# Optimization experiments

Measured on AMD Instinct MI355X. Metric: run time of the kernel, lower is better.

Reference implementation:

```python
import jax, jax.numpy as jnp
import numpy as np

B, C, REP, H, W = 4, 256, 128, 32, 128
EPS = 1e-5


def _conv1x1(x, w, b=None):
    # x: [B, Cin, H, W], w: [Cout, Cin]
    y = jnp.einsum('oc,bchw->bohw', w, x)
    if b is not None:
        y = y + b[None, :, None, None]
    return y


def _bn_train(x, gamma, beta):
    # BatchNorm2d in training mode: batch stats over (B, H, W)
    mean = jnp.mean(x, axis=(0, 2, 3), keepdims=True)
    var = jnp.var(x, axis=(0, 2, 3), keepdims=True)
    xn = (x - mean) * jax.lax.rsqrt(var + EPS)
    return gamma[None, :, None, None] * xn + beta[None, :, None, None]


def setup_inputs() -> dict:
    key = jax.random.key(0)
    ks = jax.random.split(key, 20)
    f = lambda k, s: jax.random.normal(k, s, dtype=jnp.float32)
    inp = {
        'left': f(ks[0], (B, C, H, W)),
        'right': f(ks[1], (B, C, H, W)),
        'pre_l': jax.random.uniform(ks[2], (B, 1, H, W), dtype=jnp.float32) * W,
        'pre_r': jax.random.uniform(ks[3], (B, 1, H, W), dtype=jnp.float32) * W,
        'query_l': f(ks[4], (B, REP, H, W)),
        'key_l': f(ks[5], (B, REP, H, W)),
        'query_r': f(ks[6], (B, REP, H, W)),
        'key_r': f(ks[7], (B, REP, H, W)),
        # learned 1x1-conv params (kernel stored as [Cout, Cin])
        'theta_w': f(ks[8], (REP, C + 1)) * 0.02,
        'theta_b': f(ks[9], (REP,)) * 0.02,
        'phi_w': f(ks[10], (REP, C)) * 0.02,
        'phi_b': f(ks[11], (REP,)) * 0.02,
        'g_w': f(ks[12], (REP, C)) * 0.02,
        'g_b': f(ks[13], (REP,)) * 0.02,
        'up_w': f(ks[14], (C, REP)) * 0.02,
        'up_b': f(ks[15], (C,)) * 0.02,
        'bn_gamma': f(ks[16], (C,)) * 0.1 + 1.0,
        'bn_beta': f(ks[17], (C,)) * 0.1,
    }
    return inp


def _side(x_q, x_kv, pre, query, key_feat,
          theta_w, theta_b, phi_w, phi_b, g_w, g_b,
          up_w, up_b, bn_gamma, bn_beta):
    hw = H * W
    pre = pre / W
    # theta: [B, hw, REP]
    theta = _conv1x1(jnp.concatenate([x_q, pre], axis=1), theta_w, theta_b)
    theta = theta.reshape(B, REP, hw).transpose(0, 2, 1) + \
        query.reshape(B, REP, hw).transpose(0, 2, 1)
    # phi: [B, REP, hw]
    phi = _conv1x1(x_kv, phi_w, phi_b).reshape(B, REP, hw) + \
        key_feat.reshape(B, REP, hw)
    # g: [B, hw, REP]
    g = _conv1x1(x_kv, g_w, g_b).reshape(B, REP, hw).transpose(0, 2, 1)
    # attention over all hw key positions: [B, hw, hw]
    atten = jax.nn.softmax(jnp.einsum('bqc,bck->bqk', theta, phi), axis=-1)
    # soft-argmax over key column index (arange(W) tiled H times along key axis)
    col_idx = jnp.tile(jnp.arange(W, dtype=jnp.float32), H)  # [hw]
    exp_col = jnp.einsum('bqk,k->bq', atten, col_idx)        # [B, hw]
    q_col = (jnp.arange(hw, dtype=jnp.float32) % W)[None, :]  # [1, hw]
    index = (q_col - exp_col).reshape(B, H, W)
    # value aggregation + residual projection
    after = jnp.einsum('bqk,bkc->bqc', atten, g)
    after = after.transpose(0, 2, 1).reshape(B, REP, H, W)
    out = x_q + _bn_train(_conv1x1(after, up_w, up_b), bn_gamma, bn_beta)
    return out, index


def reference(left, right, pre_l, pre_r, query_l, key_l, query_r, key_r,
              theta_w, theta_b, phi_w, phi_b, g_w, g_b,
              up_w, up_b, bn_gamma, bn_beta):
    l_n, index_l = _side(left, right, pre_l, query_l, key_r,
                         theta_w, theta_b, phi_w, phi_b, g_w, g_b,
                         up_w, up_b, bn_gamma, bn_beta)
    r_n, index_r = _side(right, left, pre_r, query_r, key_l,
                         theta_w, theta_b, phi_w, phi_b, g_w, g_b,
                         up_w, up_b, bn_gamma, bn_beta)
    return (l_n, r_n, index_l, index_r)
```

## Files before the change

### kernel.cpp

```cpp
#include <hip/hip_runtime.h>


typedef unsigned short u16;
typedef unsigned int   u32;
typedef float        floatx4 __attribute__((ext_vector_type(4)));
typedef unsigned int uintx4  __attribute__((ext_vector_type(4)));
typedef unsigned int uintx2  __attribute__((ext_vector_type(2)));
typedef _Float16     half8   __attribute__((ext_vector_type(8)));
typedef __fp16       fp16x2  __attribute__((ext_vector_type(2)));

#define HW 4096
#define CB 256
#define RP 128
#define EPSF 1e-5f

static __device__ __forceinline__ u16 f2bf(float f) {
  u32 u = __float_as_uint(f);
  u32 r = u + 0x7FFFu + ((u >> 16) & 1u);
  return (u16)(r >> 16);
}
static __device__ __forceinline__ float bf2f(u16 h) {
  return __uint_as_float(((u32)h) << 16);
}
static __device__ __forceinline__ u16 f2h(float f) {
  _Float16 h = (_Float16)f;
  return __builtin_bit_cast(u16, h);
}
static __device__ __forceinline__ float h2f(u16 h) {
  return (float)__builtin_bit_cast(_Float16, h);
}
static __device__ __forceinline__ half8 as_h8(uintx4 v) {
  return __builtin_bit_cast(half8, v);
}
static __device__ __forceinline__ u32 pkrtz(float a, float b) {
  fp16x2 h = __builtin_amdgcn_cvt_pkrtz(a, b);
  return __builtin_bit_cast(u32, h);
}
static __device__ __forceinline__ u32 pk2h(float a, float b) {
  return (u32)f2h(a) | ((u32)f2h(b) << 16);
}
static __device__ __forceinline__ void barrier_nodrain() {
  __builtin_amdgcn_sched_barrier(0);
  asm volatile("s_waitcnt lgkmcnt(0)" ::: "memory");
  __builtin_amdgcn_s_barrier();
  __builtin_amdgcn_sched_barrier(0);
}

union Pk4 { u16 u[4]; uintx2 v; };

struct ProjCfg {
  const float* x; const float* w; const float* bias;
  const float* add; const float* pre; u16* out;
  int wstride; int transposed;
};
struct ProjCfg6 { ProjCfg c[6]; };

#define XSTR 40

__global__ __launch_bounds__(256) void ra_projm(ProjCfg6 cfg, float* stz)
{
  __shared__ u16 x_lds[128 * XSTR];
  __shared__ u16 w_lds[128 * XSTR];
  if (blockIdx.x == 0) {
    ((floatx4*)stz)[threadIdx.x] = (floatx4)0.0f;
  }
  const ProjCfg C = cfg.c[blockIdx.x >> 7];
  const int inner = blockIdx.x & 127;
  const int b    = inner >> 5;
  const int pos0 = (inner & 31) * 128;
  const int tid  = threadIdx.x;
  const int wv   = tid >> 6;
  const int lane = tid & 63;
  const int ln16 = lane & 15;
  const int quad = lane >> 4;
  const int mbase = wv * 32;

  const int xc0 = (tid & 7) * 4, xp0 = (tid >> 3) * 4;
  const int wrr = tid >> 1, wch = (tid & 1) * 16;
  const bool walign = (C.wstride & 3) == 0;

  floatx4 acc[2][8];
  #pragma unroll
  for (int mt = 0; mt < 2; mt++)
    #pragma unroll
    for (int nt = 0; nt < 8; nt++) acc[mt][nt] = (floatx4)0.0f;

  floatx4 xr[4];
  floatx4 ww4[4];
  {
    #pragma unroll
    for (int i = 0; i < 4; i++)
      xr[i] = *(const floatx4*)(C.x + (size_t)(b * CB + xc0 + i) * HW + pos0 + xp0);
    const float* wp = C.w + (size_t)wrr * C.wstride + wch;
    if (walign) {
      #pragma unroll
      for (int i = 0; i < 4; i++) ww4[i] = *(const floatx4*)(wp + i * 4);
    } else {
      #pragma unroll
      for (int i = 0; i < 4; i++)
        #pragma unroll
        for (int jj = 0; jj < 4; jj++) ww4[i][jj] = wp[i * 4 + jj];
    }
  }

  #pragma unroll 1
  for (int cc = 0; cc < 8; ++cc) {
    barrier_nodrain();
    #pragma unroll
    for (int pp = 0; pp < 4; pp++) {
      uintx2 v;
      v[0] = pk2h(xr[0][pp], xr[1][pp]);
      v[1] = pk2h(xr[2][pp], xr[3][pp]);
      *(uintx2*)&x_lds[(xp0 + pp) * XSTR + xc0] = v;
    }
    {
      uintx4 v0, v1;
      v0[0] = pk2h(ww4[0][0], ww4[0][1]); v0[1] = pk2h(ww4[0][2], ww4[0][3]);
      v0[2] = pk2h(ww4[1][0], ww4[1][1]); v0[3] = pk2h(ww4[1][2], ww4[1][3]);
      v1[0] = pk2h(ww4[2][0], ww4[2][1]); v1[1] = pk2h(ww4[2][2], ww4[2][3]);
      v1[2] = pk2h(ww4[3][0], ww4[3][1]); v1[3] = pk2h(ww4[3][2], ww4[3][3]);
      *(uintx4*)&w_lds[wrr * XSTR + wch]     = v0;
      *(uintx4*)&w_lds[wrr * XSTR + wch + 8] = v1;
    }
    if (cc < 7) {
      const int c2 = (cc + 1) * 32;
      #pragma unroll
      for (int i = 0; i < 4; i++)
        xr[i] = *(const floatx4*)(C.x + (size_t)(b * CB + c2 + xc0 + i) * HW + pos0 + xp0);
      const float* wp = C.w + (size_t)wrr * C.wstride + c2 + wch;
      if (walign) {
        #pragma unroll
        for (int i = 0; i < 4; i++) ww4[i] = *(const floatx4*)(wp + i * 4);
      } else {
        #pragma unroll
        for (int i = 0; i < 4; i++)
          #pragma unroll
          for (int jj = 0; jj < 4; jj++) ww4[i][jj] = wp[i * 4 + jj];
      }
    }
    barrier_nodrain();
    if (!C.transposed) {
      half8 a0 = as_h8(*(const uintx4*)&w_lds[(mbase + ln16) * XSTR + quad * 8]);
      half8 a1 = as_h8(*(const uintx4*)&w_lds[(mbase + 16 + ln16) * XSTR + quad * 8]);
      #pragma unroll
      for (int nt = 0; nt < 8; nt++) {
        half8 bf = as_h8(*(const uintx4*)&x_lds[(nt * 16 + ln16) * XSTR + quad * 8]);
        acc[0][nt] = __builtin_amdgcn_mfma_f32_16x16x32_f16(a0, bf, acc[0][nt], 0, 0, 0);
        acc[1][nt] = __builtin_amdgcn_mfma_f32_16x16x32_f16(a1, bf, acc[1][nt], 0, 0, 0);
      }
    } else {
      half8 a0 = as_h8(*(const uintx4*)&x_lds[(mbase + ln16) * XSTR + quad * 8]);
      half8 a1 = as_h8(*(const uintx4*)&x_lds[(mbase + 16 + ln16) * XSTR + quad * 8]);
      #pragma unroll
      for (int nt = 0; nt < 8; nt++) {
        half8 bf = as_h8(*(const uintx4*)&w_lds[(nt * 16 + ln16) * XSTR + quad * 8]);
        acc[0][nt] = __builtin_amdgcn_mfma_f32_16x16x32_f16(a0, bf, acc[0][nt], 0, 0, 0);
        acc[1][nt] = __builtin_amdgcn_mfma_f32_16x16x32_f16(a1, bf, acc[1][nt], 0, 0, 0);
      }
    }
  }

  if (!C.transposed) {
    #pragma unroll
    for (int mt = 0; mt < 2; mt++) {
      const int r0 = mbase + mt * 16 + quad * 4;
      floatx4 bi = *(const floatx4*)(C.bias + r0);
      float wc[4];
      if (C.pre) {
        #pragma unroll
        for (int rr = 0; rr < 4; rr++) wc[rr] = C.w[(size_t)(r0 + rr) * C.wstride + 256];
      }
      #pragma unroll
      for (int nt = 0; nt < 8; nt++) {
        const int pos = pos0 + nt * 16 + ln16;
        floatx4 v = acc[mt][nt];
        #pragma unroll
        for (int rr = 0; rr < 4; rr++) v[rr] += bi[rr];
        if (C.pre) {
          const float pv = C.pre[(size_t)b * HW + pos] * (1.f / 128.f);
          #pragma unroll
          for (int rr = 0; rr < 4; rr++) v[rr] += pv * wc[rr];
        }
        if (C.add) {
          #pragma unroll
          for (int rr = 0; rr < 4; rr++)
            v[rr] += C.add[(size_t)(b * RP + r0 + rr) * HW + pos];
        }
        Pk4 pk;
        #pragma unroll
        for (int rr = 0; rr < 4; rr++) pk.u[rr] = f2h(v[rr]);
        *(uintx2*)(C.out + (size_t)(b * HW + pos) * RP + r0) = pk.v;
      }
    }
  } else {
    #pragma unroll
    for (int nt = 0; nt < 8; nt++) {
      const int r = nt * 16 + ln16;
      const float bs = C.bias[r];
      #pragma unroll
      for (int mt = 0; mt < 2; mt++) {
        const int pv = pos0 + mbase + mt * 16 + quad * 4;
        floatx4 v = acc[mt][nt];
        Pk4 pk;
        #pragma unroll
        for (int rr = 0; rr < 4; rr++) pk.u[rr] = f2h(v[rr] + bs);
        *(uintx2*)(C.out + (size_t)(b * RP + r) * HW + pv) = pk.v;
      }
    }
  }
}

__global__ __launch_bounds__(256) void ra_flash(
    const u16* __restrict__ thetaL, const u16* __restrict__ phiTL,
    const u16* __restrict__ gTL,
    const u16* __restrict__ thetaR, const u16* __restrict__ phiTR,
    const u16* __restrict__ gTR,
    u16* __restrict__ afterL, u16* __restrict__ afterR,
    float* __restrict__ idxL, float* __restrict__ idxR)
{
  __shared__ uintx4 phi_lds[16 * 65];
  __shared__ uintx4 g_lds[8 * 129];
  __shared__ u16 P_lds[4][16 * 76];

  const int tid  = threadIdx.x;
  const int bx   = blockIdx.x;
  const int side = bx >> 8;
  const int sbx  = bx & 255;
  const u16* __restrict__ theta = side ? thetaR : thetaL;
  const u16* __restrict__ phiT  = side ? phiTR  : phiTL;
  const u16* __restrict__ gT    = side ? gTR    : gTL;

  const int b    = sbx >> 6;
  const int q0   = (sbx & 63) * 64;
  const int wv   = tid >> 6;
  const int lane = tid & 63;
  const int ln16 = lane & 15;
  const int quad = lane >> 4;

  uintx4 aq[4];
  {
    const uintx4* tr = (const uintx4*)(theta + (size_t)(b * HW + q0 + wv * 16 + ln16) * RP);
    #pragma unroll
    for (int c = 0; c < 4; c++) aq[c] = tr[c * 4 + quad];
  }

  half8 cf0, cf1;
  {
    #pragma unroll
    for (int i = 0; i < 8; i++) {
      float c0 = (ln16 == 0) ? (float)(quad * 8 + i)      : (ln16 == 1 ? 1.f : 0.f);
      float c1 = (ln16 == 0) ? (float)(32 + quad * 8 + i) : (ln16 == 1 ? 1.f : 0.f);
      cf0[i] = (_Float16)c0;
      cf1[i] = (_Float16)c1;
    }
  }

  floatx4 accO[8];
  #pragma unroll
  for (int v = 0; v < 8; v++) accO[v] = (floatx4)0.0f;
  floatx4 accE  = (floatx4)0.0f;
  floatx4 accEo = (floatx4)0.0f;
  float m_q = -3.0e38f;

  const int sk  = tid >> 4, scb = tid & 15;
  const int gv_ = tid >> 3, gcb = tid & 7;

  uintx4 sp[4], sg[4];
  #pragma unroll
  for (int i = 0; i < 4; i++) {
    sp[i] = *(const uintx4*)(phiT + (size_t)(b * HW + i * 16 + sk) * RP + scb * 8);
    sg[i] = *(const uintx4*)(gT + (size_t)(b * RP + i * 32 + gv_) * HW + gcb * 8);
  }

  #pragma unroll 1
  for (int j = 0; j < 64; j++) {
    #pragma unroll
    for (int i = 0; i < 4; i++) {
      phi_lds[scb * 65 + i * 16 + sk] = sp[i];
      g_lds[gcb * 129 + i * 32 + gv_] = sg[i];
    }
    if (j < 63) {
      const int k0n = (j + 1) * 64;
      #pragma unroll
      for (int i = 0; i < 4; i++) {
        sp[i] = *(const uintx4*)(phiT + (size_t)(b * HW + k0n + i * 16 + sk) * RP + scb * 8);
        sg[i] = *(const uintx4*)(gT + (size_t)(b * RP + i * 32 + gv_) * HW + k0n + gcb * 8);
      }
    }
    barrier_nodrain();

    floatx4 sf[4];
    #pragma unroll
    for (int s = 0; s < 4; s++) sf[s] = (floatx4)0.0f;
    __builtin_amdgcn_s_setprio(1);
    #pragma unroll
    for (int c = 0; c < 4; c++) {
      half8 bth = as_h8(aq[c]);
      #pragma unroll
      for (int s = 0; s < 4; s++) {
        uintx4 ap = phi_lds[(c * 4 + quad) * 65 + s * 16 + ln16];
        sf[s] = __builtin_amdgcn_mfma_f32_16x16x32_f16(as_h8(ap), bth, sf[s], 0, 0, 0);
      }
    }
    __builtin_amdgcn_s_setprio(0);

    float ms0 = fmaxf(fmaxf(sf[0][0], sf[0][1]), fmaxf(sf[0][2], sf[0][3]));
    float ms1 = fmaxf(fmaxf(sf[1][0], sf[1][1]), fmaxf(sf[1][2], sf[1][3]));
    float ms2 = fmaxf(fmaxf(sf[2][0], sf[2][1]), fmaxf(sf[2][2], sf[2][3]));
    float ms3 = fmaxf(fmaxf(sf[3][0], sf[3][1]), fmaxf(sf[3][2], sf[3][3]));
    float mx = fmaxf(fmaxf(ms0, ms1), fmaxf(ms2, ms3));
    mx = fmaxf(mx, __shfl_xor(mx, 16));
    mx = fmaxf(mx, __shfl_xor(mx, 32));
    if (__any(mx > m_q + 8.f)) {
      const float mnew  = fmaxf(m_q, mx);
      const float alpha = __expf(m_q - mnew);
      m_q = mnew;
      accE *= alpha; accEo *= alpha;
      #pragma unroll
      for (int v = 0; v < 8; v++) accO[v] *= alpha;
    }
    #pragma unroll
    for (int s = 0; s < 4; s++) {
      float p0 = __expf(sf[s][0] - m_q);
      float p1 = __expf(sf[s][1] - m_q);
      float p2 = __expf(sf[s][2] - m_q);
      float p3 = __expf(sf[s][3] - m_q);
      uintx2 pkv;
      pkv[0] = pkrtz(p0, p1);
      pkv[1] = pkrtz(p2, p3);
      *(uintx2*)&P_lds[wv][ln16 * 76 + s * 16 + quad * 4] = pkv;
    }

    half8 pb0 = as_h8(*(const uintx4*)&P_lds[wv][ln16 * 76 + quad * 8]);
    half8 pb1 = as_h8(*(const uintx4*)&P_lds[wv][ln16 * 76 + 32 + quad * 8]);
    __builtin_amdgcn_s_setprio(1);
    #pragma unroll
    for (int vt = 0; vt < 8; vt++) {
      uintx4 ag0 = g_lds[quad * 129 + vt * 16 + ln16];
      uintx4 ag1 = g_lds[(4 + quad) * 129 + vt * 16 + ln16];
      accO[vt] = __builtin_amdgcn_mfma_f32_16x16x32_f16(as_h8(ag0), pb0, accO[vt], 0, 0, 0);
      accO[vt] = __builtin_amdgcn_mfma_f32_16x16x32_f16(as_h8(ag1), pb1, accO[vt], 0, 0, 0);
    }
    if (j & 1) {
      accEo = __builtin_amdgcn_mfma_f32_16x16x32_f16(cf0, pb0, accEo, 0, 0, 0);
      accEo = __builtin_amdgcn_mfma_f32_16x16x32_f16(cf1, pb1, accEo, 0, 0, 0);
    } else {
      accE  = __builtin_amdgcn_mfma_f32_16x16x32_f16(cf0, pb0, accE, 0, 0, 0);
      accE  = __builtin_amdgcn_mfma_f32_16x16x32_f16(cf1, pb1, accE, 0, 0, 0);
    }
    __builtin_amdgcn_s_setprio(0);
    barrier_nodrain();
  }

  const float l0 = accE[1] + accEo[1];
  const float a0 = accE[0] + accEo[0] + 64.f * accEo[1];
  const float l_all  = __shfl(l0, ln16);
  const float aC_all = __shfl(a0, ln16);

  const int q = q0 + wv * 16 + ln16;
  const size_t p = (size_t)b * HW + q;
  u16* after = side ? afterR : afterL;
  u16* orow = after + p * RP;
  const float invl = 1.f / l_all;
  #pragma unroll
  for (int vt = 0; vt < 8; vt++) {
    uintx2 pkv;
    pkv[0] = pkrtz(accO[vt][0] * invl, accO[vt][1] * invl);
    pkv[1] = pkrtz(accO[vt][2] * invl, accO[vt][3] * invl);
    *(uintx2*)(orow + vt * 16 + quad * 4) = pkv;
  }
  if (quad == 0) {
    float* idx = side ? idxR : idxL;
    idx[p] = (float)(q & 127) - aC_all * invl;
  }
}

#define WSTR 136

__global__ __launch_bounds__(256) void ra_upm(
    const u16* __restrict__ afterL, const u16* __restrict__ afterR,
    const float* __restrict__ w, const float* __restrict__ bias,
    u16* __restrict__ yL, u16* __restrict__ yR,
    float* __restrict__ stL, float* __restrict__ stR)
{
  __shared__ u16 w_lds[128 * WSTR];
  const int tid  = threadIdx.x;
  const int bx   = blockIdx.x;
  const int side = bx >> 8;
  const int sbx  = bx & 255;
  const u16* __restrict__ after = side ? afterR : afterL;
  u16* __restrict__ y = side ? yR : yL;
  const int b    = sbx >> 6;
  const int pos0 = ((sbx >> 1) & 31) * 128;
  const int hc   = sbx & 1;
  const int wv   = tid >> 6;
  const int lane = tid & 63;
  const int ln16 = lane & 15;
  const int quad = lane >> 4;

  {
    const int co = tid >> 1, rh = (tid & 1) * 64;
    const float* wp = w + (size_t)(hc * 128 + co) * RP + rh;
    #pragma unroll
    for (int i = 0; i < 8; i++) {
      floatx4 f0 = *(const floatx4*)(wp + i * 8);
      floatx4 f1 = *(const floatx4*)(wp + i * 8 + 4);
      uintx4 v;
      v[0] = pk2h(f0[0], f0[1]); v[1] = pk2h(f0[2], f0[3]);
      v[2] = pk2h(f1[0], f1[1]); v[3] = pk2h(f1[2], f1[3]);
      *(uintx4*)&w_lds[co * WSTR + rh + i * 8] = v;
    }
  }
  __syncthreads();

  floatx4 acc[2][8];
  #pragma unroll
  for (int mt = 0; mt < 2; mt++)
    #pragma unroll
    for (int nt = 0; nt < 8; nt++) acc[mt][nt] = (floatx4)0.0f;

  #pragma unroll
  for (int kk = 0; kk < 4; kk++) {
    half8 a[2];
    #pragma unroll
    for (int mt = 0; mt < 2; mt++)
      a[mt] = as_h8(*(const uintx4*)(after +
          (size_t)(b * HW + pos0 + wv * 32 + mt * 16 + ln16) * RP + kk * 32 + quad * 8));
    #pragma unroll
    for (int nt = 0; nt < 8; nt++) {
      half8 bf = as_h8(*(const uintx4*)&w_lds[(nt * 16 + ln16) * WSTR + kk * 32 + quad * 8]);
      acc[0][nt] = __builtin_amdgcn_mfma_f32_16x16x32_f16(a[0], bf, acc[0][nt], 0, 0, 0);
      acc[1][nt] = __builtin_amdgcn_mfma_f32_16x16x32_f16(a[1], bf, acc[1][nt], 0, 0, 0);
    }
  }

  float s_nt[8], q_nt[8];
  #pragma unroll
  for (int nt = 0; nt < 8; nt++) {
    const int co = hc * 128 + nt * 16 + ln16;
    const float bs = bias[co];
    float s = 0.f, sq = 0.f;
    #pragma unroll
    for (int mt = 0; mt < 2; mt++) {
      const int pv = pos0 + wv * 32 + mt * 16 + quad * 4;
      floatx4 v = acc[mt][nt];
      Pk4 pk;
      #pragma unroll
      for (int rr = 0; rr < 4; rr++) {
        const float yv = v[rr] + bs;
        s += yv; sq += yv * yv;
        pk.u[rr] = f2bf(yv);
      }
      *(uintx2*)(y + (size_t)(b * CB + co) * HW + pv) = pk.v;
    }
    s  += __shfl_xor(s, 16);  s  += __shfl_xor(s, 32);
    sq += __shfl_xor(sq, 16); sq += __shfl_xor(sq, 32);
    s_nt[nt] = s; q_nt[nt] = sq;
  }
  __syncthreads();
  float* scr = (float*)w_lds;
  if (quad == 0) {
    #pragma unroll
    for (int nt = 0; nt < 8; nt++) {
      scr[wv * 128 + nt * 16 + ln16]       = s_nt[nt];
      scr[512 + wv * 128 + nt * 16 + ln16] = q_nt[nt];
    }
  }
  __syncthreads();
  if (tid < 128) {
    const float s  = scr[tid] + scr[128 + tid] + scr[256 + tid] + scr[384 + tid];
    const float sq = scr[512 + tid] + scr[640 + tid] + scr[768 + tid] + scr[896 + tid];
    float* stats = side ? stR : stL;
    atomicAdd(&stats[2 * (hc * 128 + tid)], s);
    atomicAdd(&stats[2 * (hc * 128 + tid) + 1], sq);
  }
}

__global__ __launch_bounds__(256) void ra_fin(
    const float* __restrict__ left, const float* __restrict__ right,
    const u16* __restrict__ yL, const u16* __restrict__ yR,
    const float* __restrict__ stL, const float* __restrict__ stR,
    const float* __restrict__ gamma, const float* __restrict__ beta,
    float* __restrict__ out)
{
  const size_t e = (size_t)blockIdx.x * 256 + threadIdx.x;
  const int side = (int)(e >> 20);
  const size_t e4 = e & 1048575;
  const int c = (int)((e4 >> 10) & 255);
  const float* x = side ? right : left;
  const u16* y = side ? yR : yL;
  const float* stats = side ? stR : stL;
  const float s = stats[2 * c], sq = stats[2 * c + 1];
  const float mean = s * (1.f / 16384.f);
  const float var  = sq * (1.f / 16384.f) - mean * mean;
  const float rstd = rsqrtf(var + EPSF);
  const float ga = gamma[c], be = beta[c];
  floatx4 xv = ((const floatx4*)x)[e4];
  uintx2 yv = ((const uintx2*)y)[e4];
  float f0 = bf2f((u16)(yv[0] & 0xffffu));
  float f1 = bf2f((u16)(yv[0] >> 16));
  float f2 = bf2f((u16)(yv[1] & 0xffffu));
  float f3 = bf2f((u16)(yv[1] >> 16));
  floatx4 o;
  o[0] = xv[0] + ga * ((f0 - mean) * rstd) + be;
  o[1] = xv[1] + ga * ((f1 - mean) * rstd) + be;
  o[2] = xv[2] + ga * ((f2 - mean) * rstd) + be;
  o[3] = xv[3] + ga * ((f3 - mean) * rstd) + be;
  ((floatx4*)out)[(size_t)side * 1048576 + e4] = o;
}

extern "C" void kernel_launch(void* const* d_in, const int* in_sizes, int n_in,
                              void* d_out, int out_size, void* d_ws, size_t ws_size,
                              hipStream_t stream)
{
  const float* left    = (const float*)d_in[0];
  const float* right   = (const float*)d_in[1];
  const float* pre_l   = (const float*)d_in[2];
  const float* pre_r   = (const float*)d_in[3];
  const float* query_l = (const float*)d_in[4];
  const float* key_l   = (const float*)d_in[5];
  const float* query_r = (const float*)d_in[6];
  const float* key_r   = (const float*)d_in[7];
  const float* theta_w = (const float*)d_in[8];
  const float* theta_b = (const float*)d_in[9];
  const float* phi_w   = (const float*)d_in[10];
  const float* phi_b   = (const float*)d_in[11];
  const float* g_w     = (const float*)d_in[12];
  const float* g_b     = (const float*)d_in[13];
  const float* up_w    = (const float*)d_in[14];
  const float* up_b    = (const float*)d_in[15];
  const float* bn_g    = (const float*)d_in[16];
  const float* bn_b    = (const float*)d_in[17];
  float* out = (float*)d_out;

  char* ws = (char*)d_ws;
  const size_t SZ = (size_t)4 * HW * RP * 2;
  u16* thetaL = (u16*)(ws);
  u16* phiTL  = (u16*)(ws + 1 * SZ);
  u16* gTL    = (u16*)(ws + 2 * SZ);
  u16* thetaR = (u16*)(ws + 3 * SZ);
  u16* phiTR  = (u16*)(ws + 4 * SZ);
  u16* gTR    = (u16*)(ws + 5 * SZ);
  u16* afterL = (u16*)(ws + 6 * SZ);
  u16* afterR = (u16*)(ws + 7 * SZ);
  u16* yL     = (u16*)(ws + 8 * SZ);
  u16* yR     = (u16*)(ws + 10 * SZ);
  float* stL  = (float*)(ws + 12 * SZ);
  float* stR  = (float*)(ws + 12 * SZ + 2048);

  dim3 blk(256);
  ProjCfg6 pc;
  pc.c[0] = { left,  theta_w, theta_b, query_l, pre_l,   thetaL, 257, 0 };
  pc.c[1] = { right, phi_w,   phi_b,   key_r,   nullptr, phiTL,  256, 0 };
  pc.c[2] = { right, g_w,     g_b,     nullptr, nullptr, gTL,    256, 1 };
  pc.c[3] = { right, theta_w, theta_b, query_r, pre_r,   thetaR, 257, 0 };
  pc.c[4] = { left,  phi_w,   phi_b,   key_l,   nullptr, phiTR,  256, 0 };
  pc.c[5] = { left,  g_w,     g_b,     nullptr, nullptr, gTR,    256, 1 };
  ra_projm<<<768, blk, 0, stream>>>(pc, stL);

  ra_flash<<<512, blk, 0, stream>>>(thetaL, phiTL, gTL, thetaR, phiTR, gTR,
                                    afterL, afterR,
                                    out + 8388608, out + 8404992);
  ra_upm<<<512, blk, 0, stream>>>(afterL, afterR, up_w, up_b, yL, yR, stL, stR);
  ra_fin<<<8192, blk, 0, stream>>>(left, right, yL, yR, stL, stR, bn_g, bn_b, out);

  (void)in_sizes; (void)n_in; (void)out_size; (void)ws_size;
}
```

Baseline: 312.6 us.

## Recompute up-projection in BN finalize instead of storing y; swizzle flash block order

The up-projection kernel now only accumulates the BatchNorm sum and sum-of-squares. The finalize kernel recomputes the 1x1-conv GEMM from the attention output and applies the normalization and residual directly. This removes the bf16 y intermediate write and its re-read, at the cost of doing the small GEMM twice. The flash kernel's block index is also permuted so that consecutive blocks are spread across sides and batches, which may improve L2 locality or load balance across XCDs.

```diff
diff --git a/kernel.cpp b/kernel.cpp
--- a/kernel.cpp
+++ b/kernel.cpp
@@ -223,7 +223,8 @@
   __shared__ u16 P_lds[4][16 * 76];
 
   const int tid  = threadIdx.x;
-  const int bx   = blockIdx.x;
+  const int h    = blockIdx.x;
+  const int bx   = ((h & 7) << 6) | (h >> 3);
   const int side = bx >> 8;
   const int sbx  = bx & 255;
   const u16* __restrict__ theta = side ? thetaR : thetaL;
@@ -377,10 +378,9 @@
 
 #define WSTR 136
 
-__global__ __launch_bounds__(256) void ra_upm(
+__global__ __launch_bounds__(256) void ra_upstats(
     const u16* __restrict__ afterL, const u16* __restrict__ afterR,
     const float* __restrict__ w, const float* __restrict__ bias,
-    u16* __restrict__ yL, u16* __restrict__ yR,
     float* __restrict__ stL, float* __restrict__ stR)
 {
   __shared__ u16 w_lds[128 * WSTR];
@@ -389,7 +389,6 @@
   const int side = bx >> 8;
   const int sbx  = bx & 255;
   const u16* __restrict__ after = side ? afterR : afterL;
-  u16* __restrict__ y = side ? yR : yL;
   const int b    = sbx >> 6;
   const int pos0 = ((sbx >> 1) & 31) * 128;
   const int hc   = sbx & 1;
@@ -437,21 +436,15 @@
   float s_nt[8], q_nt[8];
   #pragma unroll
   for (int nt = 0; nt < 8; nt++) {
-    const int co = hc * 128 + nt * 16 + ln16;
-    const float bs = bias[co];
+    const float bs = bias[hc * 128 + nt * 16 + ln16];
     float s = 0.f, sq = 0.f;
     #pragma unroll
     for (int mt = 0; mt < 2; mt++) {
-      const int pv = pos0 + wv * 32 + mt * 16 + quad * 4;
-      floatx4 v = acc[mt][nt];
-      Pk4 pk;
       #pragma unroll
       for (int rr = 0; rr < 4; rr++) {
-        const float yv = v[rr] + bs;
+        const float yv = acc[mt][nt][rr] + bs;
         s += yv; sq += yv * yv;
-        pk.u[rr] = f2bf(yv);
-      }
-      *(uintx2*)(y + (size_t)(b * CB + co) * HW + pv) = pk.v;
+      }
     }
     s  += __shfl_xor(s, 16);  s  += __shfl_xor(s, 32);
     sq += __shfl_xor(sq, 16); sq += __shfl_xor(sq, 32);
@@ -476,37 +469,89 @@
   }
 }
 
-__global__ __launch_bounds__(256) void ra_fin(
+__global__ __launch_bounds__(256) void ra_finm(
+    const u16* __restrict__ afterL, const u16* __restrict__ afterR,
+    const float* __restrict__ w, const float* __restrict__ bias,
     const float* __restrict__ left, const float* __restrict__ right,
-    const u16* __restrict__ yL, const u16* __restrict__ yR,
     const float* __restrict__ stL, const float* __restrict__ stR,
     const float* __restrict__ gamma, const float* __restrict__ beta,
     float* __restrict__ out)
 {
-  const size_t e = (size_t)blockIdx.x * 256 + threadIdx.x;
-  const int side = (int)(e >> 20);
-  const size_t e4 = e & 1048575;
-  const int c = (int)((e4 >> 10) & 255);
+  __shared__ u16 w_lds[128 * WSTR];
+  const int tid  = threadIdx.x;
+  const int bx   = blockIdx.x;
+  const int side = bx >> 8;
+  const int sbx  = bx & 255;
+  const u16* __restrict__ after = side ? afterR : afterL;
+  const int b    = sbx >> 6;
+  const int pos0 = ((sbx >> 1) & 31) * 128;
+  const int hc   = sbx & 1;
+  const int wv   = tid >> 6;
+  const int lane = tid & 63;
+  const int ln16 = lane & 15;
+  const int quad = lane >> 4;
+
+  {
+    const int co = tid >> 1, rh = (tid & 1) * 64;
+    const float* wp = w + (size_t)(hc * 128 + co) * RP + rh;
+    #pragma unroll
+    for (int i = 0; i < 8; i++) {
+      floatx4 f0 = *(const floatx4*)(wp + i * 8);
+      floatx4 f1 = *(const floatx4*)(wp + i * 8 + 4);
+      uintx4 v;
+      v[0] = pk2h(f0[0], f0[1]); v[1] = pk2h(f0[2], f0[3]);
+      v[2] = pk2h(f1[0], f1[1]); v[3] = pk2h(f1[2], f1[3]);
+      *(uintx4*)&w_lds[co * WSTR + rh + i * 8] = v;
+    }
+  }
+  __syncthreads();
+
+  floatx4 acc[2][8];
+  #pragma unroll
+  for (int mt = 0; mt < 2; mt++)
+    #pragma unroll
+    for (int nt = 0; nt < 8; nt++) acc[mt][nt] = (floatx4)0.0f;
+
+  #pragma unroll
+  for (int kk = 0; kk < 4; kk++) {
+    half8 a[2];
+    #pragma unroll
+    for (int mt = 0; mt < 2; mt++)
+      a[mt] = as_h8(*(const uintx4*)(after +
+          (size_t)(b * HW + pos0 + wv * 32 + mt * 16 + ln16) * RP + kk * 32 + quad * 8));
+    #pragma unroll
+    for (int nt = 0; nt < 8; nt++) {
+      half8 bf = as_h8(*(const uintx4*)&w_lds[(nt * 16 + ln16) * WSTR + kk * 32 + quad * 8]);
+      acc[0][nt] = __builtin_amdgcn_mfma_f32_16x16x32_f16(a[0], bf, acc[0][nt], 0, 0, 0);
+      acc[1][nt] = __builtin_amdgcn_mfma_f32_16x16x32_f16(a[1], bf, acc[1][nt], 0, 0, 0);
+    }
+  }
+
   const float* x = side ? right : left;
-  const u16* y = side ? yR : yL;
   const float* stats = side ? stR : stL;
-  const float s = stats[2 * c], sq = stats[2 * c + 1];
-  const float mean = s * (1.f / 16384.f);
-  const float var  = sq * (1.f / 16384.f) - mean * mean;
-  const float rstd = rsqrtf(var + EPSF);
-  const float ga = gamma[c], be = beta[c];
-  floatx4 xv = ((const floatx4*)x)[e4];
-  uintx2 yv = ((const uintx2*)y)[e4];
-  float f0 = bf2f((u16)(yv[0] & 0xffffu));
-  float f1 = bf2f((u16)(yv[0] >> 16));
-  float f2 = bf2f((u16)(yv[1] & 0xffffu));
-  float f3 = bf2f((u16)(yv[1] >> 16));
-  floatx4 o;
-  o[0] = xv[0] + ga * ((f0 - mean) * rstd) + be;
-  o[1] = xv[1] + ga * ((f1 - mean) * rstd) + be;
-  o[2] = xv[2] + ga * ((f2 - mean) * rstd) + be;
-  o[3] = xv[3] + ga * ((f3 - mean) * rstd) + be;
-  ((floatx4*)out)[(size_t)side * 1048576 + e4] = o;
+  float* outs = out + (size_t)side * 4194304;
+  #pragma unroll
+  for (int nt = 0; nt < 8; nt++) {
+    const int co = hc * 128 + nt * 16 + ln16;
+    const float s = stats[2 * co], sq = stats[2 * co + 1];
+    const float mean = s * (1.f / 16384.f);
+    const float var  = sq * (1.f / 16384.f) - mean * mean;
+    const float rstd = rsqrtf(var + EPSF);
+    const float ga = gamma[co], be = beta[co];
+    const float bs = bias[co];
+    #pragma unroll
+    for (int mt = 0; mt < 2; mt++) {
+      const int pv = pos0 + wv * 32 + mt * 16 + quad * 4;
+      floatx4 xv = *(const floatx4*)(x + (size_t)(b * CB + co) * HW + pv);
+      floatx4 o;
+      #pragma unroll
+      for (int rr = 0; rr < 4; rr++) {
+        const float yv = acc[mt][nt][rr] + bs;
+        o[rr] = xv[rr] + ga * ((yv - mean) * rstd) + be;
+      }
+      *(floatx4*)(outs + (size_t)(b * CB + co) * HW + pv) = o;
+    }
+  }
 }
 
 extern "C" void kernel_launch(void* const* d_in, const int* in_sizes, int n_in,
@@ -543,10 +588,8 @@
   u16* gTR    = (u16*)(ws + 5 * SZ);
   u16* afterL = (u16*)(ws + 6 * SZ);
   u16* afterR = (u16*)(ws + 7 * SZ);
-  u16* yL     = (u16*)(ws + 8 * SZ);
-  u16* yR     = (u16*)(ws + 10 * SZ);
-  float* stL  = (float*)(ws + 12 * SZ);
-  float* stR  = (float*)(ws + 12 * SZ + 2048);
+  float* stL  = (float*)(ws + 8 * SZ);
+  float* stR  = (float*)(ws + 8 * SZ + 2048);
 
   dim3 blk(256);
   ProjCfg6 pc;
@@ -561,8 +604,9 @@
   ra_flash<<<512, blk, 0, stream>>>(thetaL, phiTL, gTL, thetaR, phiTR, gTR,
                                     afterL, afterR,
                                     out + 8388608, out + 8404992);
-  ra_upm<<<512, blk, 0, stream>>>(afterL, afterR, up_w, up_b, yL, yR, stL, stR);
-  ra_fin<<<8192, blk, 0, stream>>>(left, right, yL, yR, stL, stR, bn_g, bn_b, out);
+  ra_upstats<<<512, blk, 0, stream>>>(afterL, afterR, up_w, up_b, stL, stR);
+  ra_finm<<<512, blk, 0, stream>>>(afterL, afterR, up_w, up_b, left, right,
+                                   stL, stR, bn_g, bn_b, out);
 
   (void)in_sizes; (void)n_in; (void)out_size; (void)ws_size;
 }
```

New measurement: 313.9 us. Within noise of the previous version (+0.4%).
